# Kernel optimization log

Hardware: AMD Instinct MI355X
Metric: run time of the kernel (lower is better)

The kernel has to match this reference:

```python
import jax, jax.numpy as jnp
import numpy as np

E, K, IN_DIM, OUT_DIM = 100000, 16, 128, 128


def _linear_init(key, out_d, in_d):
    kw, kb = jax.random.split(key)
    bound = 1.0 / np.sqrt(in_d)
    W = jax.random.uniform(kw, (out_d, in_d), minval=-bound, maxval=bound, dtype=jnp.float32)
    b = jax.random.uniform(kb, (out_d,), minval=-bound, maxval=bound, dtype=jnp.float32)
    return W, b


def setup_inputs() -> dict:
    key = jax.random.key(0)
    k_feat, k_adj, k1, k2, k3, k4 = jax.random.split(key, 6)
    edge_features = jax.random.normal(k_feat, (E, IN_DIM), dtype=jnp.float32)
    edge_adjacency = jax.random.randint(k_adj, (E, K), 0, E, dtype=jnp.int64)
    mW1, mb1 = _linear_init(k1, OUT_DIM, 2 * IN_DIM)
    mW2, mb2 = _linear_init(k2, OUT_DIM, OUT_DIM)
    uW1, ub1 = _linear_init(k3, OUT_DIM, IN_DIM + OUT_DIM)
    uW2, ub2 = _linear_init(k4, OUT_DIM, OUT_DIM)
    return {"edge_features": edge_features, "edge_adjacency": edge_adjacency,
            "mW1": mW1, "mb1": mb1, "mW2": mW2, "mb2": mb2,
            "uW1": uW1, "ub1": ub1, "uW2": ub2 * 0 + ub2 if False else uW1 * 0 + uW1 if False else uW1, "ub1_": ub1} if False else {
            "edge_features": edge_features, "edge_adjacency": edge_adjacency,
            "mW1": mW1, "mb1": mb1, "mW2": mW2, "mb2": mb2,
            "uW1": uW1, "ub1": ub1, "uW2": uW2, "ub2": ub2}


def reference(edge_features, edge_adjacency, mW1, mb1, mW2, mb2, uW1, ub1, uW2, ub2):
    D = edge_features.shape[1]
    # message_net first Linear on concat([feat_i, feat_j]) split into two halves
    # to avoid materializing the [E, K, 2D] concat tensor.
    Wi, Wj = mW1[:, :D], mW1[:, D:]                      # each [O, D]
    self_part = edge_features @ Wi.T                     # [E, O]
    nbr_feat = edge_features[edge_adjacency]             # [E, K, D] gather
    h = jax.nn.relu(self_part[:, None, :] + jnp.einsum('ekd,od->eko', nbr_feat, Wj) + mb1)
    msg = jnp.einsum('eko,po->ekp', h, mW2) + mb2        # [E, K, O]
    msg = msg.mean(axis=1)                               # mean over neighbors -> [E, O]
    # update_net on concat([feat_i, msg_i]), split likewise
    Ui, Um = uW1[:, :D], uW1[:, D:]
    u = jax.nn.relu(edge_features @ Ui.T + msg @ Um.T + ub1)
    return u @ uW2.T + ub2                               # [E, O]
```

## Files before the change

kernel.cpp:

```cpp
#include <hip/hip_runtime.h>
#include <hip/hip_bf16.h>

#define NE 100000
#define NK 16
#define ND 128
#define NTILES 6250

typedef __bf16 bf16_t;
typedef bf16_t bf16x8 __attribute__((ext_vector_type(8)));
typedef bf16_t bf16x4 __attribute__((ext_vector_type(4)));
typedef float f32x4 __attribute__((ext_vector_type(4)));
typedef float f32x2 __attribute__((ext_vector_type(2)));
typedef unsigned u32x2 __attribute__((ext_vector_type(2)));
typedef unsigned short u16;
typedef unsigned char u8;

__device__ __forceinline__ u16 f2bf(float f) {
  bf16_t h = (bf16_t)f;
  return __builtin_bit_cast(u16, h);
}

__global__ void k_prep(const float* __restrict__ mW1, const float* __restrict__ uW1,
                       const float* __restrict__ uW2, const float* __restrict__ mW2,
                       const float* __restrict__ ub1, const float* __restrict__ mb2,
                       u16* __restrict__ Wi_b, u16* __restrict__ Wj_b,
                       u16* __restrict__ Ui_b, u16* __restrict__ Wp_b,
                       u16* __restrict__ W2_b, float* __restrict__ bp)
{
  const int o = blockIdx.x, t = threadIdx.x;
  Wi_b[o * ND + t] = f2bf(mW1[o * 256 + t]);
  Wj_b[o * ND + t] = f2bf(mW1[o * 256 + 128 + t]);
  Ui_b[o * ND + t] = f2bf(uW1[o * 256 + t]);
  W2_b[o * ND + t] = f2bf(uW2[o * ND + t]);
  float acc = 0.f;
  for (int p = 0; p < 128; ++p)
    acc += uW1[o * 256 + 128 + p] * mW2[p * 128 + t];
  Wp_b[o * ND + t] = f2bf(acc);
  if (t == 0) {
    float b = ub1[o];
    for (int p = 0; p < 128; ++p) b += uW1[o * 256 + 128 + p] * mb2[p];
    bp[o] = b;
  }
}

__global__ __launch_bounds__(512) void k1_szt(
    const float* __restrict__ X, const u16* __restrict__ Wi_b,
    const u16* __restrict__ Wj_b, const u16* __restrict__ Ui_b,
    const float* __restrict__ mb1, const float* __restrict__ bp,
    u8* __restrict__ Sf8, u8* __restrict__ Zf8, u16* __restrict__ Tp)
{
  __shared__ u16 xt[2][16 * ND];
  __shared__ u8  eS[2][16 * ND];
  __shared__ u8  eZ[2][16 * ND];
  __shared__ u16 eT[2][16 * ND];
  const int tid = threadIdx.x, wid = tid >> 6, lane = tid & 63;
  const int r = lane & 15, q = lane >> 4;

  bf16x8 wiF[4], wjF[4], uiF[4];
  f32x4 mbF, bpF;
  {
    const int row = wid * 16 + r;
#pragma unroll
    for (int kk = 0; kk < 4; ++kk) {
      wiF[kk] = *(const bf16x8*)(Wi_b + row * ND + kk * 32 + q * 8);
      wjF[kk] = *(const bf16x8*)(Wj_b + row * ND + kk * 32 + q * 8);
      uiF[kk] = *(const bf16x8*)(Ui_b + row * ND + kk * 32 + q * 8);
    }
    mbF = *(const f32x4*)(mb1 + wid * 16 + q * 4);
    bpF = *(const f32x4*)(bp  + wid * 16 + q * 4);
  }

  const int rs = tid >> 5, cs = tid & 31;
  const int stb = rs * 256 + ((((cs >> 1) ^ (rs & 15)) << 4) | ((cs & 1) << 3));
  const int ewb = r * 256 + ((((wid * 2 + (q >> 1)) ^ (r & 15)) << 4) | ((q & 1) << 3));
  const int ezb = r * 128 + (((wid ^ (r & 7)) << 4) | (q * 4));
  const int erow = tid >> 5, c8 = tid & 31;
  const int erb = erow * 256 + ((((c8 >> 1) ^ (erow & 15)) << 4) | ((c8 & 1) << 3));
  const int zrb = erow * 128 + ((((c8 >> 2) ^ (erow & 7)) << 4) | ((c8 & 3) << 2));

  const long stride = gridDim.x;
  long t = blockIdx.x;
  if (t >= NTILES) return;

  f32x4 xr;
  auto gload = [&](long tt) {
    xr = *(const f32x4*)(X + (tt * 16 + rs) * ND + cs * 4);
  };
  auto stage = [&](int bb) {
    bf16x4 b;
#pragma unroll
    for (int i = 0; i < 4; ++i) b[i] = (bf16_t)xr[i];
    *(bf16x4*)((char*)xt[bb] + stb) = b;
  };

  gload(t);
  stage(0);
  {
    const long t1 = t + stride;
    if (t1 < NTILES) gload(t1);
  }
  __syncthreads();
  int b = 0;

  for (; t < NTILES; t += stride) {
    const long tn = t + stride, tn2 = tn + stride;

    bf16x8 xf[4];
#pragma unroll
    for (int kk = 0; kk < 4; ++kk)
      xf[kk] = *(const bf16x8*)((const char*)xt[b] +
               r * 256 + (((kk * 4 + q) ^ (r & 15)) << 4));

    if (tn < NTILES) stage(b ^ 1);
    if (tn2 < NTILES) gload(tn2);

    f32x4 aS = {0.f, 0.f, 0.f, 0.f};
    f32x4 aZ = {0.f, 0.f, 0.f, 0.f};
    f32x4 aT = {0.f, 0.f, 0.f, 0.f};
#pragma unroll
    for (int kk = 0; kk < 4; ++kk) {
      aS = __builtin_amdgcn_mfma_f32_16x16x32_bf16(wiF[kk], xf[kk], aS, 0, 0, 0);
      aZ = __builtin_amdgcn_mfma_f32_16x16x32_bf16(wjF[kk], xf[kk], aZ, 0, 0, 0);
      aT = __builtin_amdgcn_mfma_f32_16x16x32_bf16(uiF[kk], xf[kk], aT, 0, 0, 0);
    }

    bf16x4 pT;
#pragma unroll
    for (int i = 0; i < 4; ++i) pT[i] = (bf16_t)(aT[i] + bpF[i]);
    unsigned spk = 0, zpk = 0;
    spk = __builtin_amdgcn_cvt_pk_fp8_f32(aS[0] + mbF[0], aS[1] + mbF[1], spk, false);
    spk = __builtin_amdgcn_cvt_pk_fp8_f32(aS[2] + mbF[2], aS[3] + mbF[3], spk, true);
    zpk = __builtin_amdgcn_cvt_pk_fp8_f32(aZ[0], aZ[1], zpk, false);
    zpk = __builtin_amdgcn_cvt_pk_fp8_f32(aZ[2], aZ[3], zpk, true);
    *(unsigned*)((char*)eS[b] + ezb) = spk;
    *(unsigned*)((char*)eZ[b] + ezb) = zpk;
    *(bf16x4*)((char*)eT[b] + ewb) = pT;

    __syncthreads();

    {
      const long e = t * 16 + erow;
      const unsigned vS = *(const unsigned*)((const char*)eS[b] + zrb);
      const unsigned vZ = *(const unsigned*)((const char*)eZ[b] + zrb);
      const bf16x4 vT = *(const bf16x4*)((const char*)eT[b] + erb);
      *(unsigned*)(Sf8 + e * ND + c8 * 4) = vS;
      *(unsigned*)(Zf8 + e * ND + c8 * 4) = vZ;
      *(bf16x4*)(Tp + t * 4096 + erow * 128 + c8 * 4) = vT;
    }
    b ^= 1;
  }
}

__global__ __launch_bounds__(256) void k2_gather(
    const u8* __restrict__ Zf8, const u8* __restrict__ Sf8,
    const int* __restrict__ adj, u8* __restrict__ Hf8)
{
  const int tid = threadIdx.x, w4 = tid >> 6, lane = tid & 63;
  const int q4 = lane >> 4, li = lane & 15;
  const long e = (long)blockIdx.x * 16 + w4 * 4 + q4;
  const int c0 = li * 8;

  const unsigned* sp = (const unsigned*)(Sf8 + e * ND + c0);
  const unsigned sw0 = __builtin_nontemporal_load(sp);
  const unsigned sw1 = __builtin_nontemporal_load(sp + 1);
  const f32x2 s0 = __builtin_amdgcn_cvt_pk_f32_fp8(sw0, false);
  const f32x2 s1 = __builtin_amdgcn_cvt_pk_f32_fp8(sw0, true);
  const f32x2 s2 = __builtin_amdgcn_cvt_pk_f32_fp8(sw1, false);
  const f32x2 s3 = __builtin_amdgcn_cvt_pk_f32_fp8(sw1, true);
  const float s[8] = {s0[0], s0[1], s1[0], s1[1], s2[0], s2[1], s3[0], s3[1]};

  const int myidx = __builtin_nontemporal_load(adj + e * NK + li);

  float acc[8] = {0.f, 0.f, 0.f, 0.f, 0.f, 0.f, 0.f, 0.f};
#pragma unroll
  for (int k = 0; k < NK; ++k) {
    const int n = __shfl(myidx, (lane & 48) + k);
    const u32x2 zw = *(const u32x2*)(Zf8 + (long)n * ND + c0);
    const f32x2 z0 = __builtin_amdgcn_cvt_pk_f32_fp8(zw[0], false);
    const f32x2 z1 = __builtin_amdgcn_cvt_pk_f32_fp8(zw[0], true);
    const f32x2 z2 = __builtin_amdgcn_cvt_pk_f32_fp8(zw[1], false);
    const f32x2 z3 = __builtin_amdgcn_cvt_pk_f32_fp8(zw[1], true);
    acc[0] += fmaxf(s[0] + z0[0], 0.f);
    acc[1] += fmaxf(s[1] + z0[1], 0.f);
    acc[2] += fmaxf(s[2] + z1[0], 0.f);
    acc[3] += fmaxf(s[3] + z1[1], 0.f);
    acc[4] += fmaxf(s[4] + z2[0], 0.f);
    acc[5] += fmaxf(s[5] + z2[1], 0.f);
    acc[6] += fmaxf(s[6] + z3[0], 0.f);
    acc[7] += fmaxf(s[7] + z3[1], 0.f);
  }

  unsigned h0 = 0, h1 = 0;
  h0 = __builtin_amdgcn_cvt_pk_fp8_f32(acc[0] * 0.0625f, acc[1] * 0.0625f, h0, false);
  h0 = __builtin_amdgcn_cvt_pk_fp8_f32(acc[2] * 0.0625f, acc[3] * 0.0625f, h0, true);
  h1 = __builtin_amdgcn_cvt_pk_fp8_f32(acc[4] * 0.0625f, acc[5] * 0.0625f, h1, false);
  h1 = __builtin_amdgcn_cvt_pk_fp8_f32(acc[6] * 0.0625f, acc[7] * 0.0625f, h1, true);
  unsigned* hp = (unsigned*)(Hf8 + e * ND + c0);
  __builtin_nontemporal_store(h0, hp);
  __builtin_nontemporal_store(h1, hp + 1);
}

__global__ __launch_bounds__(512) void k3_out(
    const u8* __restrict__ Hf8,
    const u16* __restrict__ Wp_b, const u16* __restrict__ W2_b,
    const float* __restrict__ ub2, float* out)
{
  __shared__ u16 ht[16 * ND];
  __shared__ u16 tt[16 * ND];
  __shared__ u16 ut[16 * ND];
  const int tid = threadIdx.x, wid = tid >> 6, lane = tid & 63;
  const int r = lane & 15, q = lane >> 4;
  const u16* tp = (const u16*)out;

  bf16x8 wpF[4], w2F[4];
  f32x4 ubF;
  {
    const int row = wid * 16 + r;
#pragma unroll
    for (int kk = 0; kk < 4; ++kk) {
      wpF[kk] = *(const bf16x8*)(Wp_b + row * ND + kk * 32 + q * 8);
      w2F[kk] = *(const bf16x8*)(W2_b + row * ND + kk * 32 + q * 8);
    }
    ubF = *(const f32x4*)(ub2 + wid * 16 + q * 4);
  }

  const int rs = tid >> 5, cs = tid & 31;
  const int stb = rs * 256 + ((((cs >> 1) ^ (rs & 15)) << 4) | ((cs & 1) << 3));
  const int trb = r * 256 + ((((wid * 2 + (q >> 1)) ^ (r & 15)) << 4) | ((q & 1) << 3));

  const long stride = gridDim.x;
  long t = blockIdx.x;
  if (t >= NTILES) return;

  unsigned hw;
  bf16x4 tr;
  auto gload = [&](long ttl) {
    hw = *(const unsigned*)(Hf8 + (ttl * 16 + rs) * ND + cs * 4);
    tr = *(const bf16x4*)(tp + ttl * 4096 + rs * 128 + cs * 4);
  };
  auto stageh = [&]() {
    const f32x2 lo = __builtin_amdgcn_cvt_pk_f32_fp8(hw, false);
    const f32x2 hi = __builtin_amdgcn_cvt_pk_f32_fp8(hw, true);
    bf16x4 hb;
    hb[0] = (bf16_t)lo[0]; hb[1] = (bf16_t)lo[1];
    hb[2] = (bf16_t)hi[0]; hb[3] = (bf16_t)hi[1];
    *(bf16x4*)((char*)ht + stb) = hb;
  };
  gload(t);
  stageh();
  *(bf16x4*)((char*)tt + stb) = tr;
  __syncthreads();

  for (; t < NTILES; t += stride) {
    const long tn = t + stride;
    if (tn < NTILES) gload(tn);

    bf16x8 hf[4];
#pragma unroll
    for (int kk = 0; kk < 4; ++kk)
      hf[kk] = *(const bf16x8*)((const char*)ht +
               r * 256 + (((kk * 4 + q) ^ (r & 15)) << 4));

    f32x4 acc;
    {
      const bf16x4 tv = *(const bf16x4*)((const char*)tt + trb);
#pragma unroll
      for (int i = 0; i < 4; ++i) acc[i] = (float)tv[i];
    }
#pragma unroll
    for (int kk = 0; kk < 4; ++kk)
      acc = __builtin_amdgcn_mfma_f32_16x16x32_bf16(wpF[kk], hf[kk], acc, 0, 0, 0);

    bf16x4 u;
#pragma unroll
    for (int i = 0; i < 4; ++i) u[i] = (bf16_t)fmaxf(acc[i], 0.f);
    const int uwb = r * 256 + ((((wid * 2 + (q >> 1)) ^ (r & 15)) << 4) | ((q & 1) << 3));

    __syncthreads();
    *(bf16x4*)((char*)ut + uwb) = u;
    if (tn < NTILES) {
      stageh();
      *(bf16x4*)((char*)tt + stb) = tr;
    }
    __syncthreads();

    bf16x8 uf[4];
#pragma unroll
    for (int kk = 0; kk < 4; ++kk)
      uf[kk] = *(const bf16x8*)((const char*)ut +
               r * 256 + (((kk * 4 + q) ^ (r & 15)) << 4));

    f32x4 o = {0.f, 0.f, 0.f, 0.f};
#pragma unroll
    for (int kk = 0; kk < 4; ++kk)
      o = __builtin_amdgcn_mfma_f32_16x16x32_bf16(w2F[kk], uf[kk], o, 0, 0, 0);
#pragma unroll
    for (int i = 0; i < 4; ++i) o[i] += ubF[i];
    *(f32x4*)(out + (t * 16 + r) * ND + wid * 16 + q * 4) = o;
  }
}

extern "C" void kernel_launch(void* const* d_in, const int* in_sizes, int n_in,
                              void* d_out, int out_size, void* d_ws, size_t ws_size,
                              hipStream_t stream)
{
  (void)in_sizes; (void)n_in; (void)out_size; (void)ws_size;
  const float* X   = (const float*)d_in[0];
  const int*   adj = (const int*)d_in[1];
  const float* mW1 = (const float*)d_in[2];
  const float* mb1 = (const float*)d_in[3];
  const float* mW2 = (const float*)d_in[4];
  const float* mb2 = (const float*)d_in[5];
  const float* uW1 = (const float*)d_in[6];
  const float* ub1 = (const float*)d_in[7];
  const float* uW2 = (const float*)d_in[8];
  const float* ub2 = (const float*)d_in[9];
  float* out = (float*)d_out;

  u8* ws8  = (u8*)d_ws;
  u8* Sf8  = ws8;
  u8* Hf8  = Sf8 + (size_t)NE * ND;
  u8* Zf8  = Hf8 + (size_t)NE * ND;
  u16* Wi_b = (u16*)(Zf8 + (size_t)NE * ND);
  u16* Wj_b = Wi_b + 128 * 128;
  u16* Ui_b = Wj_b + 128 * 128;
  u16* Wp_b = Ui_b + 128 * 128;
  u16* W2_b = Wp_b + 128 * 128;
  float* bp = (float*)(W2_b + 128 * 128);
  u16* Tp   = (u16*)d_out;

  k_prep<<<128, 128, 0, stream>>>(mW1, uW1, uW2, mW2, ub1, mb2,
                                  Wi_b, Wj_b, Ui_b, Wp_b, W2_b, bp);

  k1_szt<<<1024, 512, 0, stream>>>(X, Wi_b, Wj_b, Ui_b, mb1, bp, Sf8, Zf8, Tp);

  k2_gather<<<NTILES, 256, 0, stream>>>(Zf8, Sf8, adj, Hf8);

  k3_out<<<1024, 512, 0, stream>>>(Hf8, Wp_b, W2_b, ub2, out);
}
```

Baseline: 95.03 us.

## Fuse neighbor gather with output MLP in a persistent 32-row kernel

```diff
diff --git a/kernel.cpp b/kernel.cpp
--- a/kernel.cpp
+++ b/kernel.cpp
@@ -5,6 +5,7 @@
 #define NK 16
 #define ND 128
 #define NTILES 6250
+#define NSUP 3125
 
 typedef __bf16 bf16_t;
 typedef bf16_t bf16x8 __attribute__((ext_vector_type(8)));
@@ -18,6 +19,11 @@
 __device__ __forceinline__ u16 f2bf(float f) {
   bf16_t h = (bf16_t)f;
   return __builtin_bit_cast(u16, h);
+}
+
+__device__ __forceinline__ void soft_barrier() {
+  asm volatile("s_waitcnt lgkmcnt(0)" ::: "memory");
+  __builtin_amdgcn_s_barrier();
 }
 
 __global__ void k_prep(const float* __restrict__ mW1, const float* __restrict__ uW1,
@@ -99,7 +105,7 @@
     const long t1 = t + stride;
     if (t1 < NTILES) gload(t1);
   }
-  __syncthreads();
+  soft_barrier();
   int b = 0;
 
   for (; t < NTILES; t += stride) {
@@ -136,7 +142,7 @@
     *(unsigned*)((char*)eZ[b] + ezb) = zpk;
     *(bf16x4*)((char*)eT[b] + ewb) = pT;
 
-    __syncthreads();
+    soft_barrier();
 
     {
       const long e = t * 16 + erow;
@@ -145,72 +151,25 @@
       const bf16x4 vT = *(const bf16x4*)((const char*)eT[b] + erb);
       *(unsigned*)(Sf8 + e * ND + c8 * 4) = vS;
       *(unsigned*)(Zf8 + e * ND + c8 * 4) = vZ;
-      *(bf16x4*)(Tp + t * 4096 + erow * 128 + c8 * 4) = vT;
+      *(bf16x4*)(Tp + t * 2048 + erow * 128 + c8 * 4) = vT;
     }
     b ^= 1;
   }
 }
 
-__global__ __launch_bounds__(256) void k2_gather(
+__global__ __launch_bounds__(512) void k23_fused(
     const u8* __restrict__ Zf8, const u8* __restrict__ Sf8,
-    const int* __restrict__ adj, u8* __restrict__ Hf8)
+    const int* __restrict__ adj, const u16* __restrict__ Tp,
+    const u16* __restrict__ Wp_b, const u16* __restrict__ W2_b,
+    const float* __restrict__ ub2, float* __restrict__ out)
 {
-  const int tid = threadIdx.x, w4 = tid >> 6, lane = tid & 63;
-  const int q4 = lane >> 4, li = lane & 15;
-  const long e = (long)blockIdx.x * 16 + w4 * 4 + q4;
-  const int c0 = li * 8;
-
-  const unsigned* sp = (const unsigned*)(Sf8 + e * ND + c0);
-  const unsigned sw0 = __builtin_nontemporal_load(sp);
-  const unsigned sw1 = __builtin_nontemporal_load(sp + 1);
-  const f32x2 s0 = __builtin_amdgcn_cvt_pk_f32_fp8(sw0, false);
-  const f32x2 s1 = __builtin_amdgcn_cvt_pk_f32_fp8(sw0, true);
-  const f32x2 s2 = __builtin_amdgcn_cvt_pk_f32_fp8(sw1, false);
-  const f32x2 s3 = __builtin_amdgcn_cvt_pk_f32_fp8(sw1, true);
-  const float s[8] = {s0[0], s0[1], s1[0], s1[1], s2[0], s2[1], s3[0], s3[1]};
-
-  const int myidx = __builtin_nontemporal_load(adj + e * NK + li);
-
-  float acc[8] = {0.f, 0.f, 0.f, 0.f, 0.f, 0.f, 0.f, 0.f};
-#pragma unroll
-  for (int k = 0; k < NK; ++k) {
-    const int n = __shfl(myidx, (lane & 48) + k);
-    const u32x2 zw = *(const u32x2*)(Zf8 + (long)n * ND + c0);
-    const f32x2 z0 = __builtin_amdgcn_cvt_pk_f32_fp8(zw[0], false);
-    const f32x2 z1 = __builtin_amdgcn_cvt_pk_f32_fp8(zw[0], true);
-    const f32x2 z2 = __builtin_amdgcn_cvt_pk_f32_fp8(zw[1], false);
-    const f32x2 z3 = __builtin_amdgcn_cvt_pk_f32_fp8(zw[1], true);
-    acc[0] += fmaxf(s[0] + z0[0], 0.f);
-    acc[1] += fmaxf(s[1] + z0[1], 0.f);
-    acc[2] += fmaxf(s[2] + z1[0], 0.f);
-    acc[3] += fmaxf(s[3] + z1[1], 0.f);
-    acc[4] += fmaxf(s[4] + z2[0], 0.f);
-    acc[5] += fmaxf(s[5] + z2[1], 0.f);
-    acc[6] += fmaxf(s[6] + z3[0], 0.f);
-    acc[7] += fmaxf(s[7] + z3[1], 0.f);
-  }
-
-  unsigned h0 = 0, h1 = 0;
-  h0 = __builtin_amdgcn_cvt_pk_fp8_f32(acc[0] * 0.0625f, acc[1] * 0.0625f, h0, false);
-  h0 = __builtin_amdgcn_cvt_pk_fp8_f32(acc[2] * 0.0625f, acc[3] * 0.0625f, h0, true);
-  h1 = __builtin_amdgcn_cvt_pk_fp8_f32(acc[4] * 0.0625f, acc[5] * 0.0625f, h1, false);
-  h1 = __builtin_amdgcn_cvt_pk_fp8_f32(acc[6] * 0.0625f, acc[7] * 0.0625f, h1, true);
-  unsigned* hp = (unsigned*)(Hf8 + e * ND + c0);
-  __builtin_nontemporal_store(h0, hp);
-  __builtin_nontemporal_store(h1, hp + 1);
-}
-
-__global__ __launch_bounds__(512) void k3_out(
-    const u8* __restrict__ Hf8,
-    const u16* __restrict__ Wp_b, const u16* __restrict__ W2_b,
-    const float* __restrict__ ub2, float* out)
-{
-  __shared__ u16 ht[16 * ND];
-  __shared__ u16 tt[16 * ND];
-  __shared__ u16 ut[16 * ND];
+  __shared__ u16 ht[32 * ND];
+  __shared__ u16 tt[32 * ND];
+  __shared__ u16 ut[32 * ND];
   const int tid = threadIdx.x, wid = tid >> 6, lane = tid & 63;
   const int r = lane & 15, q = lane >> 4;
-  const u16* tp = (const u16*)out;
+  const int ew = wid * 4 + q;
+  const int c0 = r * 8;
 
   bf16x8 wpF[4], w2F[4];
   f32x4 ubF;
@@ -224,79 +183,159 @@
     ubF = *(const f32x4*)(ub2 + wid * 16 + q * 4);
   }
 
-  const int rs = tid >> 5, cs = tid & 31;
-  const int stb = rs * 256 + ((((cs >> 1) ^ (rs & 15)) << 4) | ((cs & 1) << 3));
-  const int trb = r * 256 + ((((wid * 2 + (q >> 1)) ^ (r & 15)) << 4) | ((q & 1) << 3));
+  const int hwb = ew * 256 + ((r ^ (ew & 15)) << 4);
+  const int trow = tid >> 4, tch = tid & 15;
+  const int twb = trow * 256 + ((tch ^ (trow & 15)) << 4);
+  const int uwb0 = (((wid * 2 + (q >> 1)) ^ r) << 4) | ((q & 1) << 3);
 
   const long stride = gridDim.x;
-  long t = blockIdx.x;
-  if (t >= NTILES) return;
-
-  unsigned hw;
-  bf16x4 tr;
-  auto gload = [&](long ttl) {
-    hw = *(const unsigned*)(Hf8 + (ttl * 16 + rs) * ND + cs * 4);
-    tr = *(const bf16x4*)(tp + ttl * 4096 + rs * 128 + cs * 4);
-  };
-  auto stageh = [&]() {
-    const f32x2 lo = __builtin_amdgcn_cvt_pk_f32_fp8(hw, false);
-    const f32x2 hi = __builtin_amdgcn_cvt_pk_f32_fp8(hw, true);
-    bf16x4 hb;
-    hb[0] = (bf16_t)lo[0]; hb[1] = (bf16_t)lo[1];
-    hb[2] = (bf16_t)hi[0]; hb[3] = (bf16_t)hi[1];
-    *(bf16x4*)((char*)ht + stb) = hb;
-  };
-  gload(t);
-  stageh();
-  *(bf16x4*)((char*)tt + stb) = tr;
-  __syncthreads();
-
-  for (; t < NTILES; t += stride) {
-    const long tn = t + stride;
-    if (tn < NTILES) gload(tn);
-
-    bf16x8 hf[4];
-#pragma unroll
-    for (int kk = 0; kk < 4; ++kk)
-      hf[kk] = *(const bf16x8*)((const char*)ht +
-               r * 256 + (((kk * 4 + q) ^ (r & 15)) << 4));
-
-    f32x4 acc;
+  long s = blockIdx.x;
+  if (s >= NSUP) return;
+
+  auto adjload = [&](long ss) { return adj[(ss * 32 + ew) * NK + r]; };
+
+  int myidxN;
+  float hacc[8];
+  bf16x8 trC;
+  {
+    const int myidxC = adjload(s);
+    const unsigned* sp = (const unsigned*)(Sf8 + (s * 32 + ew) * ND + c0);
+    const unsigned sw0 = sp[0], sw1 = sp[1];
+    trC = *(const bf16x8*)(Tp + s * 4096 + trow * 128 + tch * 8);
+    const long s1 = s + stride;
+    myidxN = (s1 < NSUP) ? adjload(s1) : 0;
+
+    const f32x2 a0 = __builtin_amdgcn_cvt_pk_f32_fp8(sw0, false);
+    const f32x2 a1 = __builtin_amdgcn_cvt_pk_f32_fp8(sw0, true);
+    const f32x2 a2 = __builtin_amdgcn_cvt_pk_f32_fp8(sw1, false);
+    const f32x2 a3 = __builtin_amdgcn_cvt_pk_f32_fp8(sw1, true);
+    const float sv[8] = {a0[0], a0[1], a1[0], a1[1], a2[0], a2[1], a3[0], a3[1]};
+#pragma unroll
+    for (int i = 0; i < 8; ++i) hacc[i] = 0.f;
+#pragma unroll
+    for (int k = 0; k < NK; ++k) {
+      const int n = __shfl(myidxC, (lane & 48) + k);
+      const u32x2 zw = *(const u32x2*)(Zf8 + (long)n * ND + c0);
+      const f32x2 z0 = __builtin_amdgcn_cvt_pk_f32_fp8(zw[0], false);
+      const f32x2 z1 = __builtin_amdgcn_cvt_pk_f32_fp8(zw[0], true);
+      const f32x2 z2 = __builtin_amdgcn_cvt_pk_f32_fp8(zw[1], false);
+      const f32x2 z3 = __builtin_amdgcn_cvt_pk_f32_fp8(zw[1], true);
+      hacc[0] += fmaxf(sv[0] + z0[0], 0.f);
+      hacc[1] += fmaxf(sv[1] + z0[1], 0.f);
+      hacc[2] += fmaxf(sv[2] + z1[0], 0.f);
+      hacc[3] += fmaxf(sv[3] + z1[1], 0.f);
+      hacc[4] += fmaxf(sv[4] + z2[0], 0.f);
+      hacc[5] += fmaxf(sv[5] + z2[1], 0.f);
+      hacc[6] += fmaxf(sv[6] + z3[0], 0.f);
+      hacc[7] += fmaxf(sv[7] + z3[1], 0.f);
+    }
+  }
+
+  for (; s < NSUP; s += stride) {
+    const long sn = s + stride, sn2 = sn + stride;
+    const bool hasN = (sn < NSUP);
+
     {
-      const bf16x4 tv = *(const bf16x4*)((const char*)tt + trb);
-#pragma unroll
-      for (int i = 0; i < 4; ++i) acc[i] = (float)tv[i];
-    }
-#pragma unroll
-    for (int kk = 0; kk < 4; ++kk)
-      acc = __builtin_amdgcn_mfma_f32_16x16x32_bf16(wpF[kk], hf[kk], acc, 0, 0, 0);
-
-    bf16x4 u;
-#pragma unroll
-    for (int i = 0; i < 4; ++i) u[i] = (bf16_t)fmaxf(acc[i], 0.f);
-    const int uwb = r * 256 + ((((wid * 2 + (q >> 1)) ^ (r & 15)) << 4) | ((q & 1) << 3));
-
-    __syncthreads();
-    *(bf16x4*)((char*)ut + uwb) = u;
-    if (tn < NTILES) {
-      stageh();
-      *(bf16x4*)((char*)tt + stb) = tr;
-    }
-    __syncthreads();
-
-    bf16x8 uf[4];
-#pragma unroll
-    for (int kk = 0; kk < 4; ++kk)
-      uf[kk] = *(const bf16x8*)((const char*)ut +
-               r * 256 + (((kk * 4 + q) ^ (r & 15)) << 4));
-
-    f32x4 o = {0.f, 0.f, 0.f, 0.f};
-#pragma unroll
-    for (int kk = 0; kk < 4; ++kk)
-      o = __builtin_amdgcn_mfma_f32_16x16x32_bf16(w2F[kk], uf[kk], o, 0, 0, 0);
-#pragma unroll
-    for (int i = 0; i < 4; ++i) o[i] += ubF[i];
-    *(f32x4*)(out + (t * 16 + r) * ND + wid * 16 + q * 4) = o;
+      bf16x8 hv;
+#pragma unroll
+      for (int i = 0; i < 8; ++i) hv[i] = (bf16_t)(hacc[i] * 0.0625f);
+      *(bf16x8*)((char*)ht + hwb) = hv;
+      *(bf16x8*)((char*)tt + twb) = trC;
+    }
+
+    u32x2 zbufA[8], zbufB[8];
+    unsigned swn0 = 0, swn1 = 0;
+    bf16x8 trN = {};
+    int myidxN2 = 0;
+    if (hasN) {
+#pragma unroll
+      for (int k = 0; k < 8; ++k) {
+        const int n = __shfl(myidxN, (lane & 48) + k);
+        zbufA[k] = *(const u32x2*)(Zf8 + (long)n * ND + c0);
+      }
+      const unsigned* sp = (const unsigned*)(Sf8 + (sn * 32 + ew) * ND + c0);
+      swn0 = sp[0]; swn1 = sp[1];
+      trN = *(const bf16x8*)(Tp + sn * 4096 + trow * 128 + tch * 8);
+      if (sn2 < NSUP) myidxN2 = adjload(sn2);
+    }
+
+    soft_barrier();
+
+#pragma unroll
+    for (int t2 = 0; t2 < 2; ++t2) {
+      const int rowb = (t2 * 16 + r) * 256;
+      bf16x8 hf[4];
+#pragma unroll
+      for (int kk = 0; kk < 4; ++kk)
+        hf[kk] = *(const bf16x8*)((const char*)ht + rowb + (((kk * 4 + q) ^ r) << 4));
+      f32x4 acc;
+      {
+        const bf16x4 tv = *(const bf16x4*)((const char*)tt + rowb + uwb0);
+#pragma unroll
+        for (int i = 0; i < 4; ++i) acc[i] = (float)tv[i];
+      }
+#pragma unroll
+      for (int kk = 0; kk < 4; ++kk)
+        acc = __builtin_amdgcn_mfma_f32_16x16x32_bf16(wpF[kk], hf[kk], acc, 0, 0, 0);
+      bf16x4 u;
+#pragma unroll
+      for (int i = 0; i < 4; ++i) u[i] = (bf16_t)fmaxf(acc[i], 0.f);
+      *(bf16x4*)((char*)ut + rowb + uwb0) = u;
+    }
+
+    if (hasN) {
+#pragma unroll
+      for (int k = 0; k < 8; ++k) {
+        const int n = __shfl(myidxN, (lane & 48) + 8 + k);
+        zbufB[k] = *(const u32x2*)(Zf8 + (long)n * ND + c0);
+      }
+    }
+
+    soft_barrier();
+
+#pragma unroll
+    for (int t2 = 0; t2 < 2; ++t2) {
+      const int rowb = (t2 * 16 + r) * 256;
+      bf16x8 uf[4];
+#pragma unroll
+      for (int kk = 0; kk < 4; ++kk)
+        uf[kk] = *(const bf16x8*)((const char*)ut + rowb + (((kk * 4 + q) ^ r) << 4));
+      f32x4 o = {0.f, 0.f, 0.f, 0.f};
+#pragma unroll
+      for (int kk = 0; kk < 4; ++kk)
+        o = __builtin_amdgcn_mfma_f32_16x16x32_bf16(w2F[kk], uf[kk], o, 0, 0, 0);
+#pragma unroll
+      for (int i = 0; i < 4; ++i) o[i] += ubF[i];
+      *(f32x4*)(out + (s * 32 + t2 * 16 + r) * ND + wid * 16 + q * 4) = o;
+    }
+
+    if (hasN) {
+      const f32x2 a0 = __builtin_amdgcn_cvt_pk_f32_fp8(swn0, false);
+      const f32x2 a1 = __builtin_amdgcn_cvt_pk_f32_fp8(swn0, true);
+      const f32x2 a2 = __builtin_amdgcn_cvt_pk_f32_fp8(swn1, false);
+      const f32x2 a3 = __builtin_amdgcn_cvt_pk_f32_fp8(swn1, true);
+      const float sv[8] = {a0[0], a0[1], a1[0], a1[1], a2[0], a2[1], a3[0], a3[1]};
+#pragma unroll
+      for (int i = 0; i < 8; ++i) hacc[i] = 0.f;
+#pragma unroll
+      for (int k = 0; k < 16; ++k) {
+        const u32x2 zw = (k < 8) ? zbufA[k] : zbufB[k - 8];
+        const f32x2 z0 = __builtin_amdgcn_cvt_pk_f32_fp8(zw[0], false);
+        const f32x2 z1 = __builtin_amdgcn_cvt_pk_f32_fp8(zw[0], true);
+        const f32x2 z2 = __builtin_amdgcn_cvt_pk_f32_fp8(zw[1], false);
+        const f32x2 z3 = __builtin_amdgcn_cvt_pk_f32_fp8(zw[1], true);
+        hacc[0] += fmaxf(sv[0] + z0[0], 0.f);
+        hacc[1] += fmaxf(sv[1] + z0[1], 0.f);
+        hacc[2] += fmaxf(sv[2] + z1[0], 0.f);
+        hacc[3] += fmaxf(sv[3] + z1[1], 0.f);
+        hacc[4] += fmaxf(sv[4] + z2[0], 0.f);
+        hacc[5] += fmaxf(sv[5] + z2[1], 0.f);
+        hacc[6] += fmaxf(sv[6] + z3[0], 0.f);
+        hacc[7] += fmaxf(sv[7] + z3[1], 0.f);
+      }
+      myidxN = myidxN2;
+      trC = trN;
+    }
   }
 }
 
@@ -319,22 +358,19 @@
 
   u8* ws8  = (u8*)d_ws;
   u8* Sf8  = ws8;
-  u8* Hf8  = Sf8 + (size_t)NE * ND;
-  u8* Zf8  = Hf8 + (size_t)NE * ND;
-  u16* Wi_b = (u16*)(Zf8 + (size_t)NE * ND);
+  u8* Zf8  = Sf8 + (size_t)NE * ND;
+  u16* Tp  = (u16*)(Zf8 + (size_t)NE * ND);
+  u16* Wi_b = Tp + (size_t)NE * ND;
   u16* Wj_b = Wi_b + 128 * 128;
   u16* Ui_b = Wj_b + 128 * 128;
   u16* Wp_b = Ui_b + 128 * 128;
   u16* W2_b = Wp_b + 128 * 128;
   float* bp = (float*)(W2_b + 128 * 128);
-  u16* Tp   = (u16*)d_out;
 
   k_prep<<<128, 128, 0, stream>>>(mW1, uW1, uW2, mW2, ub1, mb2,
                                   Wi_b, Wj_b, Ui_b, Wp_b, W2_b, bp);
 
   k1_szt<<<1024, 512, 0, stream>>>(X, Wi_b, Wj_b, Ui_b, mb1, bp, Sf8, Zf8, Tp);
 
-  k2_gather<<<NTILES, 256, 0, stream>>>(Zf8, Sf8, adj, Hf8);
-
-  k3_out<<<1024, 512, 0, stream>>>(Hf8, Wp_b, W2_b, ub2, out);
-}
+  k23_fused<<<1024, 512, 0, stream>>>(Zf8, Sf8, adj, Tp, Wp_b, W2_b, ub2, out);
+}
```

After: 87.54 us. 7.9% less time.

## Store S/Z/H in column-slice-major layout and gather per slice

Applied to the files above, without the earlier changes.

```diff
diff --git a/kernel.cpp b/kernel.cpp
--- a/kernel.cpp
+++ b/kernel.cpp
@@ -18,6 +18,40 @@
 __device__ __forceinline__ u16 f2bf(float f) {
   bf16_t h = (bf16_t)f;
   return __builtin_bit_cast(u16, h);
+}
+
+__device__ __forceinline__ void soft_barrier() {
+  asm volatile("s_waitcnt lgkmcnt(0)" ::: "memory");
+  __builtin_amdgcn_s_barrier();
+}
+
+__device__ __forceinline__ void unpack_s(unsigned w0, unsigned w1,
+                                         f32x4& sA, f32x4& sB) {
+  const f32x2 a0 = __builtin_amdgcn_cvt_pk_f32_fp8(w0, false);
+  const f32x2 a1 = __builtin_amdgcn_cvt_pk_f32_fp8(w0, true);
+  const f32x2 a2 = __builtin_amdgcn_cvt_pk_f32_fp8(w1, false);
+  const f32x2 a3 = __builtin_amdgcn_cvt_pk_f32_fp8(w1, true);
+  sA[0] = a0[0]; sA[1] = a0[1]; sA[2] = a1[0]; sA[3] = a1[1];
+  sB[0] = a2[0]; sB[1] = a2[1]; sB[2] = a3[0]; sB[3] = a3[1];
+}
+
+__device__ __forceinline__ void acc8(f32x4& hA, f32x4& hB,
+                                     const f32x4 sA, const f32x4 sB,
+                                     const u32x2 zw) {
+  const f32x2 z0 = __builtin_amdgcn_cvt_pk_f32_fp8(zw[0], false);
+  const f32x2 z1 = __builtin_amdgcn_cvt_pk_f32_fp8(zw[0], true);
+  const f32x2 z2 = __builtin_amdgcn_cvt_pk_f32_fp8(zw[1], false);
+  const f32x2 z3 = __builtin_amdgcn_cvt_pk_f32_fp8(zw[1], true);
+  f32x4 vA = sA, vB = sB;
+  vA[0] += z0[0]; vA[1] += z0[1]; vA[2] += z1[0]; vA[3] += z1[1];
+  vB[0] += z2[0]; vB[1] += z2[1]; vB[2] += z3[0]; vB[3] += z3[1];
+#pragma unroll
+  for (int i = 0; i < 4; ++i) {
+    vA[i] = fmaxf(vA[i], 0.f);
+    vB[i] = fmaxf(vB[i], 0.f);
+  }
+  hA += vA;
+  hB += vB;
 }
 
 __global__ void k_prep(const float* __restrict__ mW1, const float* __restrict__ uW1,
@@ -47,7 +81,7 @@
     const float* __restrict__ X, const u16* __restrict__ Wi_b,
     const u16* __restrict__ Wj_b, const u16* __restrict__ Ui_b,
     const float* __restrict__ mb1, const float* __restrict__ bp,
-    u8* __restrict__ Sf8, u8* __restrict__ Zf8, u16* __restrict__ Tp)
+    u8* __restrict__ Ss, u8* __restrict__ Zs, u16* __restrict__ Tp)
 {
   __shared__ u16 xt[2][16 * ND];
   __shared__ u8  eS[2][16 * ND];
@@ -76,7 +110,8 @@
   const int ezb = r * 128 + (((wid ^ (r & 7)) << 4) | (q * 4));
   const int erow = tid >> 5, c8 = tid & 31;
   const int erb = erow * 256 + ((((c8 >> 1) ^ (erow & 15)) << 4) | ((c8 & 1) << 3));
-  const int zrb = erow * 128 + ((((c8 >> 2) ^ (erow & 7)) << 4) | ((c8 & 3) << 2));
+  const int st8 = tid >> 6, es = (tid >> 2) & 15, cq = tid & 3;
+  const int slb = es * 128 + (((st8 ^ (es & 7)) << 4) | (cq << 2));
 
   const long stride = gridDim.x;
   long t = blockIdx.x;
@@ -99,7 +134,7 @@
     const long t1 = t + stride;
     if (t1 < NTILES) gload(t1);
   }
-  __syncthreads();
+  soft_barrier();
   int b = 0;
 
   for (; t < NTILES; t += stride) {
@@ -136,81 +171,73 @@
     *(unsigned*)((char*)eZ[b] + ezb) = zpk;
     *(bf16x4*)((char*)eT[b] + ewb) = pT;
 
-    __syncthreads();
+    soft_barrier();
 
     {
-      const long e = t * 16 + erow;
-      const unsigned vS = *(const unsigned*)((const char*)eS[b] + zrb);
-      const unsigned vZ = *(const unsigned*)((const char*)eZ[b] + zrb);
+      const unsigned vS = *(const unsigned*)((const char*)eS[b] + slb);
+      const unsigned vZ = *(const unsigned*)((const char*)eZ[b] + slb);
       const bf16x4 vT = *(const bf16x4*)((const char*)eT[b] + erb);
-      *(unsigned*)(Sf8 + e * ND + c8 * 4) = vS;
-      *(unsigned*)(Zf8 + e * ND + c8 * 4) = vZ;
-      *(bf16x4*)(Tp + t * 4096 + erow * 128 + c8 * 4) = vT;
+      const size_t so = (size_t)st8 * (NE * 16) + (t * 16 + es) * 16 + cq * 4;
+      *(unsigned*)(Ss + so) = vS;
+      *(unsigned*)(Zs + so) = vZ;
+      *(bf16x4*)(Tp + t * 2048 + erow * 128 + c8 * 4) = vT;
     }
     b ^= 1;
   }
 }
 
-__global__ __launch_bounds__(256) void k2_gather(
-    const u8* __restrict__ Zf8, const u8* __restrict__ Sf8,
-    const int* __restrict__ adj, u8* __restrict__ Hf8)
-{
-  const int tid = threadIdx.x, w4 = tid >> 6, lane = tid & 63;
-  const int q4 = lane >> 4, li = lane & 15;
-  const long e = (long)blockIdx.x * 16 + w4 * 4 + q4;
-  const int c0 = li * 8;
-
-  const unsigned* sp = (const unsigned*)(Sf8 + e * ND + c0);
-  const unsigned sw0 = __builtin_nontemporal_load(sp);
-  const unsigned sw1 = __builtin_nontemporal_load(sp + 1);
-  const f32x2 s0 = __builtin_amdgcn_cvt_pk_f32_fp8(sw0, false);
-  const f32x2 s1 = __builtin_amdgcn_cvt_pk_f32_fp8(sw0, true);
-  const f32x2 s2 = __builtin_amdgcn_cvt_pk_f32_fp8(sw1, false);
-  const f32x2 s3 = __builtin_amdgcn_cvt_pk_f32_fp8(sw1, true);
-  const float s[8] = {s0[0], s0[1], s1[0], s1[1], s2[0], s2[1], s3[0], s3[1]};
-
-  const int myidx = __builtin_nontemporal_load(adj + e * NK + li);
-
-  float acc[8] = {0.f, 0.f, 0.f, 0.f, 0.f, 0.f, 0.f, 0.f};
+__global__ __launch_bounds__(256) void k2_slice(
+    const u8* __restrict__ Zs, const u8* __restrict__ Ss,
+    const int* __restrict__ adj, u8* __restrict__ Hs)
+{
+  const int tid = threadIdx.x, lane = tid & 63, wv = tid >> 6;
+  const int s = blockIdx.x & 7;
+  const long tb = blockIdx.x >> 3;
+  const int p = lane & 1;
+  const long e = tb * 128 + wv * 32 + (lane >> 1);
+  if (e >= NE) return;
+  const size_t sb = (size_t)s * (NE * 16);
+
+  const int* ar = adj + e * NK + p * 8;
+  const int4 ia = *(const int4*)(ar);
+  const int4 ib = *(const int4*)(ar + 4);
+
+  const u32x2 sw = *(const u32x2*)(Ss + sb + e * 16 + p * 8);
+  f32x4 sA, sB;
+  unpack_s(sw[0], sw[1], sA, sB);
+
+  f32x4 hA = {0.f, 0.f, 0.f, 0.f}, hB = {0.f, 0.f, 0.f, 0.f};
+  const int base = lane & ~1;
 #pragma unroll
   for (int k = 0; k < NK; ++k) {
-    const int n = __shfl(myidx, (lane & 48) + k);
-    const u32x2 zw = *(const u32x2*)(Zf8 + (long)n * ND + c0);
-    const f32x2 z0 = __builtin_amdgcn_cvt_pk_f32_fp8(zw[0], false);
-    const f32x2 z1 = __builtin_amdgcn_cvt_pk_f32_fp8(zw[0], true);
-    const f32x2 z2 = __builtin_amdgcn_cvt_pk_f32_fp8(zw[1], false);
-    const f32x2 z3 = __builtin_amdgcn_cvt_pk_f32_fp8(zw[1], true);
-    acc[0] += fmaxf(s[0] + z0[0], 0.f);
-    acc[1] += fmaxf(s[1] + z0[1], 0.f);
-    acc[2] += fmaxf(s[2] + z1[0], 0.f);
-    acc[3] += fmaxf(s[3] + z1[1], 0.f);
-    acc[4] += fmaxf(s[4] + z2[0], 0.f);
-    acc[5] += fmaxf(s[5] + z2[1], 0.f);
-    acc[6] += fmaxf(s[6] + z3[0], 0.f);
-    acc[7] += fmaxf(s[7] + z3[1], 0.f);
+    const int el = k & 7;
+    const int src = el == 0 ? ia.x : el == 1 ? ia.y : el == 2 ? ia.z :
+                    el == 3 ? ia.w : el == 4 ? ib.x : el == 5 ? ib.y :
+                    el == 6 ? ib.z : ib.w;
+    const int n = __shfl(src, base | (k >> 3));
+    const u32x2 zw = *(const u32x2*)(Zs + sb + (size_t)n * 16 + p * 8);
+    acc8(hA, hB, sA, sB, zw);
   }
 
   unsigned h0 = 0, h1 = 0;
-  h0 = __builtin_amdgcn_cvt_pk_fp8_f32(acc[0] * 0.0625f, acc[1] * 0.0625f, h0, false);
-  h0 = __builtin_amdgcn_cvt_pk_fp8_f32(acc[2] * 0.0625f, acc[3] * 0.0625f, h0, true);
-  h1 = __builtin_amdgcn_cvt_pk_fp8_f32(acc[4] * 0.0625f, acc[5] * 0.0625f, h1, false);
-  h1 = __builtin_amdgcn_cvt_pk_fp8_f32(acc[6] * 0.0625f, acc[7] * 0.0625f, h1, true);
-  unsigned* hp = (unsigned*)(Hf8 + e * ND + c0);
-  __builtin_nontemporal_store(h0, hp);
-  __builtin_nontemporal_store(h1, hp + 1);
+  h0 = __builtin_amdgcn_cvt_pk_fp8_f32(hA[0] * 0.0625f, hA[1] * 0.0625f, h0, false);
+  h0 = __builtin_amdgcn_cvt_pk_fp8_f32(hA[2] * 0.0625f, hA[3] * 0.0625f, h0, true);
+  h1 = __builtin_amdgcn_cvt_pk_fp8_f32(hB[0] * 0.0625f, hB[1] * 0.0625f, h1, false);
+  h1 = __builtin_amdgcn_cvt_pk_fp8_f32(hB[2] * 0.0625f, hB[3] * 0.0625f, h1, true);
+  u32x2 hv; hv[0] = h0; hv[1] = h1;
+  *(u32x2*)(Hs + sb + e * 16 + p * 8) = hv;
 }
 
 __global__ __launch_bounds__(512) void k3_out(
-    const u8* __restrict__ Hf8,
+    const u8* __restrict__ Hs, const u16* __restrict__ Tp,
     const u16* __restrict__ Wp_b, const u16* __restrict__ W2_b,
-    const float* __restrict__ ub2, float* out)
+    const float* __restrict__ ub2, float* __restrict__ out)
 {
   __shared__ u16 ht[16 * ND];
   __shared__ u16 tt[16 * ND];
   __shared__ u16 ut[16 * ND];
   const int tid = threadIdx.x, wid = tid >> 6, lane = tid & 63;
   const int r = lane & 15, q = lane >> 4;
-  const u16* tp = (const u16*)out;
 
   bf16x8 wpF[4], w2F[4];
   f32x4 ubF;
@@ -235,21 +262,24 @@
   unsigned hw;
   bf16x4 tr;
   auto gload = [&](long ttl) {
-    hw = *(const unsigned*)(Hf8 + (ttl * 16 + rs) * ND + cs * 4);
-    tr = *(const bf16x4*)(tp + ttl * 4096 + rs * 128 + cs * 4);
+    hw = *(const unsigned*)(Hs + (size_t)(cs >> 2) * (NE * 16) +
+                            (ttl * 16 + rs) * 16 + (cs & 3) * 4);
+    tr = *(const bf16x4*)(Tp + ttl * 2048 + rs * 128 + cs * 4);
   };
+  const int hsb = rs * 256 + ((((cs >> 2) ^ (rs & 15)) << 4) | ((cs & 3) << 3)) / 1;
   auto stageh = [&]() {
     const f32x2 lo = __builtin_amdgcn_cvt_pk_f32_fp8(hw, false);
     const f32x2 hi = __builtin_amdgcn_cvt_pk_f32_fp8(hw, true);
     bf16x4 hb;
     hb[0] = (bf16_t)lo[0]; hb[1] = (bf16_t)lo[1];
     hb[2] = (bf16_t)hi[0]; hb[3] = (bf16_t)hi[1];
-    *(bf16x4*)((char*)ht + stb) = hb;
+    const int wb = rs * 256 + ((((cs >> 1) ^ (rs & 15)) << 4) | ((cs & 1) << 3));
+    *(bf16x4*)((char*)ht + wb) = hb;
   };
   gload(t);
   stageh();
   *(bf16x4*)((char*)tt + stb) = tr;
-  __syncthreads();
+  soft_barrier();
 
   for (; t < NTILES; t += stride) {
     const long tn = t + stride;
@@ -276,13 +306,13 @@
     for (int i = 0; i < 4; ++i) u[i] = (bf16_t)fmaxf(acc[i], 0.f);
     const int uwb = r * 256 + ((((wid * 2 + (q >> 1)) ^ (r & 15)) << 4) | ((q & 1) << 3));
 
-    __syncthreads();
+    soft_barrier();
     *(bf16x4*)((char*)ut + uwb) = u;
     if (tn < NTILES) {
       stageh();
       *(bf16x4*)((char*)tt + stb) = tr;
     }
-    __syncthreads();
+    soft_barrier();
 
     bf16x8 uf[4];
 #pragma unroll
@@ -318,23 +348,24 @@
   float* out = (float*)d_out;
 
   u8* ws8  = (u8*)d_ws;
-  u8* Sf8  = ws8;
-  u8* Hf8  = Sf8 + (size_t)NE * ND;
-  u8* Zf8  = Hf8 + (size_t)NE * ND;
-  u16* Wi_b = (u16*)(Zf8 + (size_t)NE * ND);
+  u8* Ss   = ws8;
+  u8* Zs   = Ss + (size_t)NE * ND;
+  u8* Hs   = Zs + (size_t)NE * ND;
+  u16* Tp  = (u16*)(Hs + (size_t)NE * ND);
+  u16* Wi_b = Tp + (size_t)NE * ND;
   u16* Wj_b = Wi_b + 128 * 128;
   u16* Ui_b = Wj_b + 128 * 128;
   u16* Wp_b = Ui_b + 128 * 128;
   u16* W2_b = Wp_b + 128 * 128;
   float* bp = (float*)(W2_b + 128 * 128);
-  u16* Tp   = (u16*)d_out;
 
   k_prep<<<128, 128, 0, stream>>>(mW1, uW1, uW2, mW2, ub1, mb2,
                                   Wi_b, Wj_b, Ui_b, Wp_b, W2_b, bp);
 
-  k1_szt<<<1024, 512, 0, stream>>>(X, Wi_b, Wj_b, Ui_b, mb1, bp, Sf8, Zf8, Tp);
-
-  k2_gather<<<NTILES, 256, 0, stream>>>(Zf8, Sf8, adj, Hf8);
-
-  k3_out<<<1024, 512, 0, stream>>>(Hf8, Wp_b, W2_b, ub2, out);
-}
+  k1_szt<<<1024, 512, 0, stream>>>(X, Wi_b, Wj_b, Ui_b, mb1, bp, Ss, Zs, Tp);
+
+  const int nb2 = 8 * ((NE + 127) / 128);
+  k2_slice<<<nb2, 256, 0, stream>>>(Zs, Ss, adj, Hs);
+
+  k3_out<<<1024, 512, 0, stream>>>(Hs, Tp, Wp_b, W2_b, ub2, out);
+}
```

After: 117.6 us. 23.8% more time.
